# Kernel tuning notes

Hardware: AMD Instinct MI355X
Metric: run time of the kernel (lower is better)

## Reference

```python
import jax, jax.numpy as jnp
import numpy as np

B, S, D_MODEL = 8, 1024, 512
DIM_K = DIM_V = 512
N_HEADS = 8
DK = DIM_K // N_HEADS
DV = DIM_V // N_HEADS
NORM = 1.0 / np.sqrt(D_MODEL).astype(np.float32)  # note: 1/sqrt(d_model), per source


def setup_inputs() -> dict:
    key = jax.random.key(0)
    ks = jax.random.split(key, 6)
    s = 0.05  # small init to keep softmax well-conditioned
    return {
        "x": jax.random.normal(ks[0], (B, S, D_MODEL), jnp.float32),
        "y": jax.random.normal(ks[1], (B, S, D_MODEL), jnp.float32),
        "q_w": jax.random.normal(ks[2], (D_MODEL, DIM_K), jnp.float32) * s,
        "q_b": jnp.zeros((DIM_K,), jnp.float32),
        "k_w": jax.random.normal(ks[3], (D_MODEL, DIM_K), jnp.float32) * s,
        "k_b": jnp.zeros((DIM_K,), jnp.float32),
        "v_w": jax.random.normal(ks[4], (D_MODEL, DIM_V), jnp.float32) * s,
        "v_b": jnp.zeros((DIM_V,), jnp.float32),
        "o_w": jax.random.normal(ks[5], (DIM_V, D_MODEL), jnp.float32) * s,
        "o_b": jnp.zeros((D_MODEL,), jnp.float32),
    }


def reference(x, y, q_w, q_b, k_w, k_b, v_w, v_b, o_w, o_b):
    b, s, _ = x.shape
    # Faithful to torch: plain row-major reshape (B,S,dim) -> (H,B,S,dh),
    # NOT a per-token head split.
    Q = (x @ q_w + q_b).reshape(N_HEADS, b, s, DK)
    K = (y @ k_w + k_b).reshape(N_HEADS, b, s, DK)
    V = (y @ v_w + v_b).reshape(N_HEADS, b, s, DV)
    scores = jnp.einsum("hbqd,hbkd->hbqk", Q, K) * NORM  # [H,B,S,S]
    # dynamic mean-threshold mask: keep only scores strictly above row mean
    thre = jnp.mean(scores, axis=-1, keepdims=True)
    scores = jnp.where(scores > thre, scores, -jnp.inf)
    attn = jax.nn.softmax(scores, axis=-1)
    out = jnp.einsum("hbqk,hbkd->hbqd", attn, V).reshape(b, s, DIM_V)
    return out @ o_w + o_b
```

## Files before the change

### kernel.cpp

```cpp
#include <hip/hip_runtime.h>
#include <hip/hip_bf16.h>
#include <hip/hip_fp16.h>


typedef _Float16 f16;
typedef __attribute__((ext_vector_type(4))) _Float16 f16x4;
typedef __attribute__((ext_vector_type(8))) _Float16 f16x8;
typedef __attribute__((ext_vector_type(8))) short bf16x8;
typedef __attribute__((ext_vector_type(4))) float f32x4;

#define MFMA16(a, b, c) __builtin_amdgcn_mfma_f32_16x16x32_f16((a), (b), (c), 0, 0, 0)
#define MFMAB16(a, b, c) __builtin_amdgcn_mfma_f32_16x16x32_bf16((a), (b), (c), 0, 0, 0)
#define MFMAPV(a, b, c) __builtin_amdgcn_mfma_f32_16x16x16f16((a), (b), (c), 0, 0, 0)

#if defined(__has_builtin) && __has_builtin(__builtin_amdgcn_exp2f)
#define EXPFN(x) __builtin_amdgcn_exp2f(x)
#define QPROJ_SCALE (0.04419417382415922f * 1.4426950408889634f)
#else
#define EXPFN(x) __expf(x)
#define QPROJ_SCALE 0.04419417382415922f
#endif

#define GLL16(gp, lp)                                       \
  __builtin_amdgcn_global_load_lds(                         \
      (const __attribute__((address_space(1))) void*)(gp),  \
      (__attribute__((address_space(3))) void*)(lp), 16, 0, 0)

__device__ __forceinline__ float b2f(short s) {
  return __uint_as_float(((unsigned)(unsigned short)s) << 16);
}

__device__ __forceinline__ void splitbf(float v, short& h, short& l) {
  unsigned short hu = __bfloat16_as_ushort(__float2bfloat16(v));
  h = (short)hu;
  float hf = __uint_as_float(((unsigned)hu) << 16);
  l = (short)__bfloat16_as_ushort(__float2bfloat16(v - hf));
}

__global__ void k_wt(const float* __restrict__ w0, const float* __restrict__ w1,
                     const float* __restrict__ w2, const float* __restrict__ w3,
                     short* __restrict__ qh, short* __restrict__ ql,
                     short* __restrict__ kh, short* __restrict__ kl,
                     f16* __restrict__ vt, f16* __restrict__ ot) {
  const float* W;
  switch (blockIdx.z) {
    case 0: W = w0; break;
    case 1: W = w1; break;
    case 2: W = w2; break;
    default: W = w3; break;
  }
  __shared__ float t[32][33];
  int bx = blockIdx.x, by = blockIdx.y;
  int tx = threadIdx.x, ty = threadIdx.y;
#pragma unroll
  for (int i = 0; i < 32; i += 8)
    t[ty + i][tx] = W[(size_t)(by * 32 + ty + i) * 512 + bx * 32 + tx];
  __syncthreads();
#pragma unroll
  for (int i = 0; i < 32; i += 8) {
    size_t idx = (size_t)(bx * 32 + ty + i) * 512 + by * 32 + tx;
    float v = t[tx][ty + i];
    if (blockIdx.z < 2) {
      short h, l;
      splitbf(v, h, l);
      if (blockIdx.z == 0) { qh[idx] = h; ql[idx] = l; }
      else { kh[idx] = h; kl[idx] = l; }
    } else {
      if (blockIdx.z == 2) vt[idx] = (f16)v;
      else ot[idx] = (f16)v;
    }
  }
}

__global__ __launch_bounds__(256) void k_split(
    const float* __restrict__ x, const float* __restrict__ y,
    short* __restrict__ Xh, short* __restrict__ Xl, short* __restrict__ Yh,
    short* __restrict__ Yl, f16* __restrict__ Ym) {
  const float* src = blockIdx.y ? y : x;
  short* dh = blockIdx.y ? Yh : Xh;
  short* dl = blockIdx.y ? Yl : Xl;
  const size_t i = ((size_t)blockIdx.x * 256 + threadIdx.x) * 8;
  float4 a = *(const float4*)(src + i);
  float4 b = *(const float4*)(src + i + 4);
  float v[8] = {a.x, a.y, a.z, a.w, b.x, b.y, b.z, b.w};
  bf16x8 h, l;
#pragma unroll
  for (int j = 0; j < 8; ++j) {
    short hh, ll;
    splitbf(v[j], hh, ll);
    h[j] = hh;
    l[j] = ll;
  }
  *(bf16x8*)(dh + i) = h;
  *(bf16x8*)(dl + i) = l;
  if (blockIdx.y) {
    f16x8 m8;
#pragma unroll
    for (int j = 0; j < 8; ++j) m8[j] = (f16)v[j];
    *(f16x8*)(Ym + i) = m8;
  }
}

template <typename OT>
__device__ __forceinline__ void gemm16_gll(const f16* __restrict__ A,
                                           const f16* __restrict__ WT,
                                           const float* __restrict__ bias,
                                           OT* __restrict__ C, int m0, int n0,
                                           f16 (*As)[32], f16 (*Bs)[32]) {
  const int tid = threadIdx.x;
  const int wv = tid >> 6, lane = tid & 63;
  const int wm = wv >> 1, wn = wv & 1;
  const int l15 = lane & 15, lg = lane >> 4;
  const int srow = lane >> 2, sslot = lane & 3;

  const f16* gsb = (wv < 2) ? A : WT;
  const int rb = (wv < 2) ? m0 : n0;
  f16(*ldsb)[32] = (wv < 2) ? As : Bs;
  const int half = (wv & 1) * 64;

  const f32x4 fz = {0.f, 0.f, 0.f, 0.f};
  f32x4 acc[4][4];
#pragma unroll
  for (int m = 0; m < 4; ++m)
#pragma unroll
    for (int n = 0; n < 4; ++n) acc[m][n] = fz;

  for (int k0 = 0; k0 < 512; k0 += 32) {
    __syncthreads();
#pragma unroll
    for (int j = 0; j < 4; ++j) {
      const int row = half + j * 16 + srow;
      const int slog = sslot ^ ((row >> 1) & 3);
      GLL16(gsb + (size_t)(rb + row) * 512 + k0 + slog * 8,
            &ldsb[half + j * 16][0]);
    }
    __syncthreads();
    f16x8 af[4], bf[4];
#pragma unroll
    for (int m = 0; m < 4; ++m) {
      const int r = wm * 64 + m * 16 + l15;
      af[m] = *(const f16x8*)&As[r][(lg ^ ((r >> 1) & 3)) * 8];
    }
#pragma unroll
    for (int n = 0; n < 4; ++n) {
      const int r = wn * 64 + n * 16 + l15;
      bf[n] = *(const f16x8*)&Bs[r][(lg ^ ((r >> 1) & 3)) * 8];
    }
#pragma unroll
    for (int m = 0; m < 4; ++m)
#pragma unroll
      for (int n = 0; n < 4; ++n) acc[m][n] = MFMA16(af[m], bf[n], acc[m][n]);
  }
#pragma unroll
  for (int n = 0; n < 4; ++n) {
    const int col = n0 + wn * 64 + n * 16 + l15;
    const float b = bias[col];
#pragma unroll
    for (int m = 0; m < 4; ++m) {
      const int row = m0 + wm * 64 + m * 16 + lg * 4;
#pragma unroll
      for (int r = 0; r < 4; ++r)
        C[(size_t)(row + r) * 512 + col] = (OT)(acc[m][n][r] + b);
    }
  }
}

__global__ __launch_bounds__(256) void k_gemm_out(const f16* __restrict__ Om,
                                                  const f16* __restrict__ owT,
                                                  const float* __restrict__ ob,
                                                  float* __restrict__ out) {
  __shared__ __align__(16) f16 As[128][32];
  __shared__ __align__(16) f16 Bs[128][32];
  gemm16_gll<float>(Om, owT, ob, out, blockIdx.y * 128, blockIdx.x * 128, As,
                    Bs);
}

__global__ __launch_bounds__(256) void k_proj(
    const short* __restrict__ Xh, const short* __restrict__ Xl,
    const short* __restrict__ Yh, const short* __restrict__ Yl,
    const f16* __restrict__ Ym, const short* __restrict__ qwh,
    const short* __restrict__ qwl, const short* __restrict__ kwh,
    const short* __restrict__ kwl, const f16* __restrict__ vwT,
    const float* __restrict__ qb, const float* __restrict__ kbias,
    const float* __restrict__ vb, short* __restrict__ Qh,
    short* __restrict__ Ql, short* __restrict__ Kh, short* __restrict__ Kl,
    f16* __restrict__ Vm, float* __restrict__ Kpart) {
  __shared__ __align__(16) short sm4[4][128][32];
  const int m0 = blockIdx.y * 128, n0 = blockIdx.x * 128;
  const int z = blockIdx.z;
  if (z == 2) {
    gemm16_gll<f16>(Ym, vwT, vb, Vm, m0, n0, (f16(*)[32]) & sm4[0][0][0],
                    (f16(*)[32]) & sm4[1][0][0]);
    return;
  }
  const short* Agh = z ? Yh : Xh;
  const short* Agl = z ? Yl : Xl;
  const short* Wh = z ? kwh : qwh;
  const short* Wl = z ? kwl : qwl;
  const float* bias = z ? kbias : qb;
  short* Ch = z ? Kh : Qh;
  short* Cl = z ? Kl : Ql;
  const float osc = z ? 1.f : (float)QPROJ_SCALE;

  const int tid = threadIdx.x;
  const int wv = tid >> 6, lane = tid & 63;
  const int wm = wv >> 1, wn = wv & 1;
  const int l15 = lane & 15, lg = lane >> 4;
  const int srow = lane >> 2, sslot = lane & 3;

  const short* gsb = (wv == 0) ? Agh : (wv == 1) ? Agl : (wv == 2) ? Wh : Wl;
  const int rb = (wv < 2) ? m0 : n0;
  short(*ldsb)[32] = sm4[wv];
  short(*Ah)[32] = sm4[0];
  short(*Al)[32] = sm4[1];
  short(*Bh)[32] = sm4[2];
  short(*Bl)[32] = sm4[3];

  const f32x4 fz = {0.f, 0.f, 0.f, 0.f};
  f32x4 acc[4][4];
#pragma unroll
  for (int m = 0; m < 4; ++m)
#pragma unroll
    for (int n = 0; n < 4; ++n) acc[m][n] = fz;

  for (int k0 = 0; k0 < 512; k0 += 32) {
    __syncthreads();
#pragma unroll
    for (int j = 0; j < 8; ++j) {
      const int row = j * 16 + srow;
      const int slog = sslot ^ ((row >> 1) & 3);
      GLL16(gsb + (size_t)(rb + row) * 512 + k0 + slog * 8, &ldsb[j * 16][0]);
    }
    __syncthreads();
    bf16x8 afh[4], afl[4], bfh[4], bfl[4];
#pragma unroll
    for (int m = 0; m < 4; ++m) {
      const int r = wm * 64 + m * 16 + l15;
      const int sl = (lg ^ ((r >> 1) & 3)) * 8;
      afh[m] = *(const bf16x8*)&Ah[r][sl];
      afl[m] = *(const bf16x8*)&Al[r][sl];
    }
#pragma unroll
    for (int n = 0; n < 4; ++n) {
      const int r = wn * 64 + n * 16 + l15;
      const int sl = (lg ^ ((r >> 1) & 3)) * 8;
      bfh[n] = *(const bf16x8*)&Bh[r][sl];
      bfl[n] = *(const bf16x8*)&Bl[r][sl];
    }
#pragma unroll
    for (int m = 0; m < 4; ++m)
#pragma unroll
      for (int n = 0; n < 4; ++n) {
        acc[m][n] = MFMAB16(afh[m], bfh[n], acc[m][n]);
        acc[m][n] = MFMAB16(afh[m], bfl[n], acc[m][n]);
        acc[m][n] = MFMAB16(afl[m], bfh[n], acc[m][n]);
      }
  }
  float csum[4];
#pragma unroll
  for (int n = 0; n < 4; ++n) {
    const int col = n0 + wn * 64 + n * 16 + l15;
    const float b = bias[col];
    csum[n] = 16.f * b;
#pragma unroll
    for (int m = 0; m < 4; ++m) {
      const int row = m0 + wm * 64 + m * 16 + lg * 4;
#pragma unroll
      for (int r = 0; r < 4; ++r) {
        const float vraw = acc[m][n][r] + b;
        csum[n] += acc[m][n][r];
        short h, l;
        splitbf(vraw * osc, h, l);
        const size_t idx = (size_t)(row + r) * 512 + col;
        Ch[idx] = h;
        Cl[idx] = l;
      }
    }
  }
  if (z == 1) {
    float* cred = (float*)&sm4[0][0][0];
    __syncthreads();
#pragma unroll
    for (int n = 0; n < 4; ++n)
      cred[(wn * 64 + n * 16 + l15) * 8 + wm * 4 + lg] = csum[n];
    __syncthreads();
    if (tid < 64) {
      float s = 0.f;
#pragma unroll
      for (int j = 0; j < 8; ++j)
        s += cred[tid * 8 + j] + cred[(tid + 64) * 8 + j];
      Kpart[((size_t)blockIdx.y * 4 + blockIdx.x) * 64 + tid] = s;
    }
  }
}

__global__ __launch_bounds__(256) void k_vtr(const f16* __restrict__ Vm,
                                             f16* __restrict__ Vt) {
  const int p = blockIdx.y;
  const int j0 = blockIdx.x * 16;
  __shared__ f16 L[16][520];
  const int tid = threadIdx.x;
#pragma unroll
  for (int it = 0; it < 4; ++it) {
    int idx = it * 256 + tid;
    int row = idx >> 6, oct = idx & 63;
    *(f16x8*)&L[row][oct * 8] =
        *(const f16x8*)&Vm[(size_t)(p * 128 + j0 + row) * 512 + oct * 8];
  }
  __syncthreads();
#pragma unroll
  for (int it = 0; it < 4; ++it) {
    int idx = it * 256 + tid;
    int dh = idx >> 4, j = idx & 15;
    f16x8 v;
#pragma unroll
    for (int g = 0; g < 8; ++g) v[g] = L[j][g * 64 + dh];
    *(f16x8*)&Vt[((size_t)p * 64 + dh) * 1024 + (j0 + j) * 8] = v;
  }
}

#define LOADREG(cc)                              \
  {                                              \
    rh = *(const bf16x8*)(KhSrc + (cc) * 4096);  \
    rl = *(const bf16x8*)(KlSrc + (cc) * 4096);  \
    rv = *(const f16x8*)(VSrc + (cc) * 64);      \
  }
#define STOREBUF(b)                      \
  {                                      \
    *(bf16x8*)&KhS[b][skey][sslot] = rh; \
    *(bf16x8*)&KlS[b][skey][sslot] = rl; \
    *(f16x8*)&Vs[b][skey][sslot] = rv;   \
  }

__global__ __launch_bounds__(512, 4) void k_attn(
    const short* __restrict__ Qh, const short* __restrict__ Ql,
    const short* __restrict__ Kh, const short* __restrict__ Kl,
    const f16* __restrict__ Vt, const float* __restrict__ Kpart,
    f16* __restrict__ Om) {
  constexpr int S = 1024, DH = 64;
  const int p = blockIdx.x;
  const int qt = blockIdx.y;
  const size_t pb = (size_t)p * S * DH;
  const short* Qhp = Qh + pb;
  const short* Qlp = Ql + pb;
  const short* Khp = Kh + pb;
  const short* Klp = Kl + pb;
  const f16* Vtp = Vt + pb;
  f16* Op = Om + pb;

  const int tid = threadIdx.x;
  const int w = tid >> 6, lane = tid & 63;
  const int l15 = lane & 15, lg = lane >> 4;

  __shared__ __align__(16) short KhS[2][64][64];
  __shared__ __align__(16) short KlS[2][64][64];
  __shared__ __align__(16) f16 Vs[2][64][64];

  const int skey = tid >> 3;
  const int slot8 = tid & 7;
  const int sslot = (slot8 ^ (skey & 7)) * 8;
  const short* KhSrc = Khp + skey * 64 + slot8 * 8;
  const short* KlSrc = Klp + skey * 64 + slot8 * 8;
  const f16* VSrc = Vtp + (size_t)skey * 1024 + slot8 * 8;

  bf16x8 rh, rl;
  f16x8 rv;
  LOADREG(0);
  STOREBUF(0);
  LOADREG(1);

  const int qrow = qt * 128 + w * 16;
  const size_t qo = (size_t)(qrow + l15) * DH + lg * 8;
  bf16x8 qh0 = *(const bf16x8*)(Qhp + qo);
  bf16x8 ql0 = *(const bf16x8*)(Qlp + qo);
  bf16x8 qh1 = *(const bf16x8*)(Qhp + qo + 32);
  bf16x8 ql1 = *(const bf16x8*)(Qlp + qo + 32);

  const float* kp = Kpart + (size_t)p * 256;
  float km0[8], km1[8];
#pragma unroll
  for (int j = 0; j < 8; ++j) { km0[j] = 0.f; km1[j] = 0.f; }
#pragma unroll
  for (int pt = 0; pt < 4; ++pt) {
    const float* bb = kp + pt * 64;
#pragma unroll
    for (int j = 0; j < 8; ++j) {
      km0[j] += bb[lg * 8 + j];
      km1[j] += bb[32 + lg * 8 + j];
    }
  }
  float sm = 0.f;
#pragma unroll
  for (int j = 0; j < 8; ++j) {
    sm += (b2f(qh0[j]) + b2f(ql0[j])) * km0[j] +
          (b2f(qh1[j]) + b2f(ql1[j])) * km1[j];
  }
  sm += __shfl_xor(sm, 16);
  sm += __shfl_xor(sm, 32);
  sm *= (1.f / 1024.f);

  const f32x4 fz = {0.f, 0.f, 0.f, 0.f};
  const f16x4 kones = {(f16)1.f, (f16)1.f, (f16)1.f, (f16)1.f};
  f32x4 oac[4];
#pragma unroll
  for (int d = 0; d < 4; ++d) oac[d] = fz;
  f32x4 od = fz;

  for (int c = 0; c < 16; ++c) {
    __syncthreads();
    const int cb = c & 1;
    if (c < 15) STOREBUF(cb ^ 1);
    if (c < 14) LOADREG(c + 2);
    __builtin_amdgcn_s_setprio(1);
#pragma unroll
    for (int t = 0; t < 4; ++t) {
      const int krow = t * 16 + l15;
      const int ksw = krow & 7;
      bf16x8 kh0 = *(const bf16x8*)&KhS[cb][krow][(lg ^ ksw) * 8];
      bf16x8 kh1 = *(const bf16x8*)&KhS[cb][krow][((4 + lg) ^ ksw) * 8];
      bf16x8 kl0 = *(const bf16x8*)&KlS[cb][krow][(lg ^ ksw) * 8];
      bf16x8 kl1 = *(const bf16x8*)&KlS[cb][krow][((4 + lg) ^ ksw) * 8];
      f32x4 a = fz;
      a = MFMAB16(kh0, qh0, a);
      a = MFMAB16(kh1, qh1, a);
      a = MFMAB16(kh0, ql0, a);
      a = MFMAB16(kl0, qh0, a);
      a = MFMAB16(kh1, ql1, a);
      a = MFMAB16(kl1, qh1, a);
      f16x4 pf;
#pragma unroll
      for (int r = 0; r < 4; ++r) {
        float v = a[r];
        float e = (v > sm) ? EXPFN(v) : 0.f;
        pf[r] = (f16)e;
      }
      od = MFMAPV(kones, pf, od);
#pragma unroll
      for (int d0 = 0; d0 < 4; ++d0) {
        const int vrow = d0 * 16 + l15;
        const int vsw = vrow & 7;
        f16x4 va = *(const f16x4*)&Vs[cb][vrow]
                                     [(((t * 2 + (lg >> 1)) ^ vsw) * 8) +
                                      (lg & 1) * 4];
        oac[d0] = MFMAPV(va, pf, oac[d0]);
      }
    }
    __builtin_amdgcn_s_setprio(0);
  }

  const float inv = 1.f / od[0];
#pragma unroll
  for (int d0 = 0; d0 < 4; ++d0) {
    f16x4 o0;
#pragma unroll
    for (int r = 0; r < 4; ++r) o0[r] = (f16)(oac[d0][r] * inv);
    *(f16x4*)&Op[(size_t)(qrow + l15) * DH + d0 * 16 + lg * 4] = o0;
  }
}

extern "C" void kernel_launch(void* const* d_in, const int* in_sizes, int n_in,
                              void* d_out, int out_size, void* d_ws,
                              size_t ws_size, hipStream_t stream) {
  const float* x = (const float*)d_in[0];
  const float* y = (const float*)d_in[1];
  const float* qw = (const float*)d_in[2];
  const float* qb = (const float*)d_in[3];
  const float* kw = (const float*)d_in[4];
  const float* kbias = (const float*)d_in[5];
  const float* vw = (const float*)d_in[6];
  const float* vb = (const float*)d_in[7];
  const float* ow = (const float*)d_in[8];
  const float* ob = (const float*)d_in[9];
  float* out = (float*)d_out;

  char* ws = (char*)d_ws;
  const size_t WT_B = 512ull * 512 * 2;
  const size_t MAT_B = 8192ull * 512 * 2;
  short* qwhT = (short*)(ws + 0 * WT_B);
  short* qwlT = (short*)(ws + 1 * WT_B);
  short* kwhT = (short*)(ws + 2 * WT_B);
  short* kwlT = (short*)(ws + 3 * WT_B);
  f16* vwT = (f16*)(ws + 4 * WT_B);
  f16* owT = (f16*)(ws + 5 * WT_B);
  char* m = ws + 6 * WT_B;
  short* Qh = (short*)(m + 0 * MAT_B);
  short* Ql = (short*)(m + 1 * MAT_B);
  short* Kh = (short*)(m + 2 * MAT_B);
  short* Kl = (short*)(m + 3 * MAT_B);
  f16* Vm = (f16*)(m + 4 * MAT_B);
  short* Xh = (short*)(m + 5 * MAT_B);
  short* Xl = (short*)(m + 6 * MAT_B);
  short* Yh = (short*)(m + 7 * MAT_B);
  short* Yl = (short*)(m + 8 * MAT_B);
  f16* Ym = (f16*)(m + 9 * MAT_B);
  float* Kpart = (float*)(m + 10 * MAT_B);
  f16* Vtr = (f16*)Xh;
  f16* Om = (f16*)Yh;

  hipLaunchKernelGGL(k_wt, dim3(16, 16, 4), dim3(32, 8), 0, stream, qw, kw, vw,
                     ow, qwhT, qwlT, kwhT, kwlT, vwT, owT);
  hipLaunchKernelGGL(k_split, dim3(2048, 2), dim3(256), 0, stream, x, y, Xh,
                     Xl, Yh, Yl, Ym);
  hipLaunchKernelGGL(k_proj, dim3(4, 64, 3), dim3(256), 0, stream, Xh, Xl, Yh,
                     Yl, Ym, qwhT, qwlT, kwhT, kwlT, vwT, qb, kbias, vb, Qh,
                     Ql, Kh, Kl, Vm, Kpart);
  hipLaunchKernelGGL(k_vtr, dim3(8, 64), dim3(256), 0, stream, Vm, Vtr);
  hipLaunchKernelGGL(k_attn, dim3(64, 8), dim3(512), 0, stream, Qh, Ql, Kh, Kl,
                     Vtr, Kpart, Om);
  hipLaunchKernelGGL(k_gemm_out, dim3(4, 64), dim3(256), 0, stream, Om, owT,
                     ob, out);
}
```

Baseline: 141.6 us.

## Double-buffer LDS staging in projection/output GEMMs and swizzle block order

The projection and output GEMMs now use two LDS buffers, so the global→LDS loads for the next K-slice are issued while MFMAs run on the current one. This drops one barrier per iteration and aims to hide load latency. Block indices are also remapped with a swizzle so neighbouring blocks share tiles in cache. The cost is doubled LDS per block (64KB for k_proj), which can lower occupancy, and correctness relies on the barrier waiting for the async loads.

Result: faster. 118.9 us (-16.0%).

```diff
diff --git a/kernel.cpp b/kernel.cpp
--- a/kernel.cpp
+++ b/kernel.cpp
@@ -101,12 +101,24 @@
   }
 }
 
+#define GSTAGE(buf, kk)                                              \
+  {                                                                  \
+    _Pragma("unroll") for (int j = 0; j < 4; ++j) {                  \
+      const int rowu = half + j * 16;                                \
+      const int row = rowu + srow;                                   \
+      const int slog = sslot ^ ((row >> 1) & 3);                     \
+      GLL16(gsb + (size_t)(rb + row) * 512 + (kk) + slog * 8,        \
+            &ldsb[buf][rowu][0]);                                    \
+    }                                                                \
+  }
+
 template <typename OT>
 __device__ __forceinline__ void gemm16_gll(const f16* __restrict__ A,
                                            const f16* __restrict__ WT,
                                            const float* __restrict__ bias,
                                            OT* __restrict__ C, int m0, int n0,
-                                           f16 (*As)[32], f16 (*Bs)[32]) {
+                                           f16 (*As)[128][32],
+                                           f16 (*Bs)[128][32]) {
   const int tid = threadIdx.x;
   const int wv = tid >> 6, lane = tid & 63;
   const int wm = wv >> 1, wn = wv & 1;
@@ -115,7 +127,7 @@
 
   const f16* gsb = (wv < 2) ? A : WT;
   const int rb = (wv < 2) ? m0 : n0;
-  f16(*ldsb)[32] = (wv < 2) ? As : Bs;
+  f16(*ldsb)[128][32] = (wv < 2) ? As : Bs;
   const int half = (wv & 1) * 64;
 
   const f32x4 fz = {0.f, 0.f, 0.f, 0.f};
@@ -125,31 +137,27 @@
 #pragma unroll
     for (int n = 0; n < 4; ++n) acc[m][n] = fz;
 
+  GSTAGE(0, 0);
+  int cur = 0;
   for (int k0 = 0; k0 < 512; k0 += 32) {
     __syncthreads();
-#pragma unroll
-    for (int j = 0; j < 4; ++j) {
-      const int row = half + j * 16 + srow;
-      const int slog = sslot ^ ((row >> 1) & 3);
-      GLL16(gsb + (size_t)(rb + row) * 512 + k0 + slog * 8,
-            &ldsb[half + j * 16][0]);
-    }
-    __syncthreads();
+    if (k0 < 480) GSTAGE(cur ^ 1, k0 + 32);
     f16x8 af[4], bf[4];
 #pragma unroll
     for (int m = 0; m < 4; ++m) {
       const int r = wm * 64 + m * 16 + l15;
-      af[m] = *(const f16x8*)&As[r][(lg ^ ((r >> 1) & 3)) * 8];
+      af[m] = *(const f16x8*)&As[cur][r][(lg ^ ((r >> 1) & 3)) * 8];
     }
 #pragma unroll
     for (int n = 0; n < 4; ++n) {
       const int r = wn * 64 + n * 16 + l15;
-      bf[n] = *(const f16x8*)&Bs[r][(lg ^ ((r >> 1) & 3)) * 8];
+      bf[n] = *(const f16x8*)&Bs[cur][r][(lg ^ ((r >> 1) & 3)) * 8];
     }
 #pragma unroll
     for (int m = 0; m < 4; ++m)
 #pragma unroll
       for (int n = 0; n < 4; ++n) acc[m][n] = MFMA16(af[m], bf[n], acc[m][n]);
+    cur ^= 1;
   }
 #pragma unroll
   for (int n = 0; n < 4; ++n) {
@@ -169,11 +177,23 @@
                                                   const f16* __restrict__ owT,
                                                   const float* __restrict__ ob,
                                                   float* __restrict__ out) {
-  __shared__ __align__(16) f16 As[128][32];
-  __shared__ __align__(16) f16 Bs[128][32];
-  gemm16_gll<float>(Om, owT, ob, out, blockIdx.y * 128, blockIdx.x * 128, As,
+  __shared__ __align__(16) f16 As[2][128][32];
+  __shared__ __align__(16) f16 Bs[2][128][32];
+  const int lid = blockIdx.x + (blockIdx.y << 2);
+  const int swz = ((lid & 7) << 5) + (lid >> 3);
+  gemm16_gll<float>(Om, owT, ob, out, (swz >> 2) * 128, (swz & 3) * 128, As,
                     Bs);
 }
+
+#define PSTAGE(buf, kk)                                             \
+  {                                                                 \
+    _Pragma("unroll") for (int j = 0; j < 8; ++j) {                 \
+      const int row = j * 16 + srow;                                \
+      const int slog = sslot ^ ((row >> 1) & 3);                    \
+      GLL16(gsb + (size_t)(rb + row) * 512 + (kk) + slog * 8,       \
+            &sm4[buf][wv][j * 16][0]);                              \
+    }                                                               \
+  }
 
 __global__ __launch_bounds__(256) void k_proj(
     const short* __restrict__ Xh, const short* __restrict__ Xl,
@@ -185,12 +205,15 @@
     const float* __restrict__ vb, short* __restrict__ Qh,
     short* __restrict__ Ql, short* __restrict__ Kh, short* __restrict__ Kl,
     f16* __restrict__ Vm, float* __restrict__ Kpart) {
-  __shared__ __align__(16) short sm4[4][128][32];
-  const int m0 = blockIdx.y * 128, n0 = blockIdx.x * 128;
+  __shared__ __align__(16) short sm4[2][4][128][32];
+  const int lid = blockIdx.x + (blockIdx.y << 2);
+  const int swz = ((lid & 7) << 5) + (lid >> 3);
+  const int nt = swz & 3, mt = swz >> 2;
+  const int m0 = mt * 128, n0 = nt * 128;
   const int z = blockIdx.z;
   if (z == 2) {
-    gemm16_gll<f16>(Ym, vwT, vb, Vm, m0, n0, (f16(*)[32]) & sm4[0][0][0],
-                    (f16(*)[32]) & sm4[1][0][0]);
+    gemm16_gll<f16>(Ym, vwT, vb, Vm, m0, n0, (f16(*)[128][32]) & sm4[0][0][0][0],
+                    (f16(*)[128][32]) & sm4[0][2][0][0]);
     return;
   }
   const short* Agh = z ? Yh : Xh;
@@ -210,11 +233,6 @@
 
   const short* gsb = (wv == 0) ? Agh : (wv == 1) ? Agl : (wv == 2) ? Wh : Wl;
   const int rb = (wv < 2) ? m0 : n0;
-  short(*ldsb)[32] = sm4[wv];
-  short(*Ah)[32] = sm4[0];
-  short(*Al)[32] = sm4[1];
-  short(*Bh)[32] = sm4[2];
-  short(*Bl)[32] = sm4[3];
 
   const f32x4 fz = {0.f, 0.f, 0.f, 0.f};
   f32x4 acc[4][4];
@@ -223,29 +241,25 @@
 #pragma unroll
     for (int n = 0; n < 4; ++n) acc[m][n] = fz;
 
+  PSTAGE(0, 0);
+  int cur = 0;
   for (int k0 = 0; k0 < 512; k0 += 32) {
     __syncthreads();
-#pragma unroll
-    for (int j = 0; j < 8; ++j) {
-      const int row = j * 16 + srow;
-      const int slog = sslot ^ ((row >> 1) & 3);
-      GLL16(gsb + (size_t)(rb + row) * 512 + k0 + slog * 8, &ldsb[j * 16][0]);
-    }
-    __syncthreads();
+    if (k0 < 480) PSTAGE(cur ^ 1, k0 + 32);
     bf16x8 afh[4], afl[4], bfh[4], bfl[4];
 #pragma unroll
     for (int m = 0; m < 4; ++m) {
       const int r = wm * 64 + m * 16 + l15;
       const int sl = (lg ^ ((r >> 1) & 3)) * 8;
-      afh[m] = *(const bf16x8*)&Ah[r][sl];
-      afl[m] = *(const bf16x8*)&Al[r][sl];
+      afh[m] = *(const bf16x8*)&sm4[cur][0][r][sl];
+      afl[m] = *(const bf16x8*)&sm4[cur][1][r][sl];
     }
 #pragma unroll
     for (int n = 0; n < 4; ++n) {
       const int r = wn * 64 + n * 16 + l15;
       const int sl = (lg ^ ((r >> 1) & 3)) * 8;
-      bfh[n] = *(const bf16x8*)&Bh[r][sl];
-      bfl[n] = *(const bf16x8*)&Bl[r][sl];
+      bfh[n] = *(const bf16x8*)&sm4[cur][2][r][sl];
+      bfl[n] = *(const bf16x8*)&sm4[cur][3][r][sl];
     }
 #pragma unroll
     for (int m = 0; m < 4; ++m)
@@ -255,6 +269,7 @@
         acc[m][n] = MFMAB16(afh[m], bfl[n], acc[m][n]);
         acc[m][n] = MFMAB16(afl[m], bfh[n], acc[m][n]);
       }
+    cur ^= 1;
   }
   float csum[4];
 #pragma unroll
@@ -278,7 +293,7 @@
     }
   }
   if (z == 1) {
-    float* cred = (float*)&sm4[0][0][0];
+    float* cred = (float*)&sm4[0][0][0][0];
     __syncthreads();
 #pragma unroll
     for (int n = 0; n < 4; ++n)
@@ -289,7 +304,7 @@
 #pragma unroll
       for (int j = 0; j < 8; ++j)
         s += cred[tid * 8 + j] + cred[(tid + 64) * 8 + j];
-      Kpart[((size_t)blockIdx.y * 4 + blockIdx.x) * 64 + tid] = s;
+      Kpart[((size_t)mt * 4 + nt) * 64 + tid] = s;
     }
   }
 }
```
